# Kernel optimization log

Hardware: AMD Instinct MI355X
Metric: run time of the kernel (lower is better)

## Reference

```python
import jax, jax.numpy as jnp
import numpy as np

TRUNC = (24, 24, 24)
OUT = (32, 32, 32)


def setup_inputs() -> dict:
    key = jax.random.key(0)
    x = jax.random.normal(key, (8, 32, 48, 48, 48), dtype=jnp.float32)
    return {"x": x}


def reference(x):
    # "DCT" as implemented in the source: real part of an ortho-normalized 3D FFT
    x_dct = jnp.real(jnp.fft.fftn(x, axes=(2, 3, 4), norm='ortho'))
    # crop to low-frequency corner, zero-pad up to output_size
    x_crop = x_dct[:, :, :TRUNC[0], :TRUNC[1], :TRUNC[2]]
    pad = ((0, 0), (0, 0),
           (0, OUT[0] - TRUNC[0]),
           (0, OUT[1] - TRUNC[1]),
           (0, OUT[2] - TRUNC[2]))
    x_pad = jnp.pad(x_crop, pad)
    # inverse transform on the output_size grid, keep real part
    x_idct = jnp.real(jnp.fft.ifftn(x_pad, axes=(2, 3, 4), norm='ortho'))
    return x_idct
```

## Files before the change

### kernel.cpp

```cpp
#include <hip/hip_runtime.h>
#include <math.h>


#define TWO_PI_48 0.13089969389957470f
#define TWO_PI_32 0.19634954084936207f
#define NORM_F    1.6611664e-05f

typedef _Float16 half8  __attribute__((ext_vector_type(8)));
typedef _Float16 half4v __attribute__((ext_vector_type(4)));
typedef float    f32x4  __attribute__((ext_vector_type(4)));

__device__ _Float16 T1frag[2][3][2][64][8];
__device__ _Float16 T2frag[2][3][2][64][8];
__device__ __align__(16) _Float16 TK2frag[2][4][3][64][8];
__device__ __align__(16) _Float16 MB2frag[2][4][2][64][8];
__device__ __align__(16) _Float16 TB3frag[2][2][2][64][8];

__device__ int g_twdone = 0;

__global__ void k_init_tw() {
  if (g_twdone) return;
  const int idx = blockIdx.x * 256 + threadIdx.x;
  if (idx < 3072) {
    const int j  = idx & 7;
    const int l  = (idx >> 3) & 63;
    const int ks = (idx >> 9) & 1;
    const int t  = idx >> 10;
    const int k  = ks * 32 + (l >> 4) * 8 + j;
    {
      const int m = t * 16 + (l & 15);
      float v = 0.f;
      if (k < 48) {
        const float a = (float)(((m % 24) * k) % 48) * TWO_PI_48;
        v = (m < 24) ? cosf(a) : -sinf(a);
      }
      const _Float16 h = (_Float16)v;
      T1frag[0][t][ks][l][j] = h;
      T1frag[1][t][ks][l][j] = (_Float16)(v - (float)h);
    }
    {
      const int c = t * 16 + (l & 15);
      float v = 0.f;
      if (k < 48) {
        const float a = (float)(((c % 24) * k) % 48) * TWO_PI_48;
        v = (c < 24) ? cosf(a) : sinf(a);
      }
      const _Float16 h = (_Float16)v;
      T2frag[0][t][ks][l][j] = h;
      T2frag[1][t][ks][l][j] = (_Float16)(v - (float)h);
    }
  } else if (idx < 3072 + 6144) {
    const int local = idx - 3072;
    const int j = local & 7, l = (local >> 3) & 63;
    const int rest = local >> 9;
    const int ks = rest % 3, mt = rest / 3;
    const int m   = mt * 16 + (l & 15);
    const int kap = ks * 32 + (l >> 4) * 8 + j;
    const int n1  = kap % 48;
    const bool isVi = kap >= 48;
    const int m1  = m & 31;
    const bool isWi = m >= 32;
    float acc = 0.f;
    for (int k1 = 0; k1 < 24; ++k1) {
      float s32v, c32v, s48v, c48v;
      sincosf((float)((k1 * m1) % 32) * TWO_PI_32, &s32v, &c32v);
      sincosf((float)((k1 * n1) % 48) * TWO_PI_48, &s48v, &c48v);
      acc = fmaf(isWi ? s32v : c32v, isVi ? s48v : c48v, acc);
    }
    const _Float16 h = (_Float16)acc;
    TK2frag[0][mt][ks][l][j] = h;
    TK2frag[1][mt][ks][l][j] = (_Float16)(acc - (float)h);
  } else if (idx < 3072 + 6144 + 4096) {
    const int local = idx - (3072 + 6144);
    const int j = local & 7, l = (local >> 3) & 63;
    const int rest = local >> 9;
    const int ks = rest & 1, mt = rest >> 1;
    const int m   = mt * 16 + (l & 15);
    const int kap = ks * 32 + (l >> 4) * 8 + j;
    float v = 0.f;
    if (kap < 48) {
      const int k2 = kap % 24;
      const int m2 = m & 31;
      float s, c;
      sincosf((float)((k2 * m2) % 32) * TWO_PI_32, &s, &c);
      if (m < 32) v = (kap < 24) ? c : -s;
      else        v = (kap < 24) ? s :  c;
    }
    const _Float16 h = (_Float16)v;
    MB2frag[0][mt][ks][l][j] = h;
    MB2frag[1][mt][ks][l][j] = (_Float16)(v - (float)h);
  } else if (idx < 15360) {
    const int local = idx - (3072 + 6144 + 4096);
    const int j = local & 7, l = (local >> 3) & 63;
    const int rest = local >> 9;
    const int ks = rest & 1, nt = rest >> 1;
    const int m3  = nt * 16 + (l & 15);
    const int kap = ks * 32 + (l >> 4) * 8 + j;
    float v = 0.f;
    if (kap < 48) {
      const int k3 = kap % 24;
      float s, c;
      sincosf((float)((k3 * m3) % 32) * TWO_PI_32, &s, &c);
      v = (kap < 24) ? c : -s;
    }
    const _Float16 h = (_Float16)v;
    TB3frag[0][nt][ks][l][j] = h;
    TB3frag[1][nt][ks][l][j] = (_Float16)(v - (float)h);
  }
}

__device__ inline void split8(const float* qf, half8& h, half8& lo) {
#pragma unroll
  for (int j = 0; j < 8; ++j) {
    const _Float16 hh = (_Float16)qf[j];
    h[j]  = hh;
    lo[j] = (_Float16)(qf[j] - (float)hh);
  }
}

__global__ __launch_bounds__(192) void k_a12_mfma(const float* __restrict__ x,
                                                  float2* __restrict__ V) {
  const int bx   = blockIdx.x;
  const int bc   = blockIdx.y;
  const int tid  = threadIdx.x;
  const int lane = tid & 63;
  const int w    = tid >> 6;

  __shared__ __align__(16) unsigned char arenaA[13824];
  __shared__ __align__(16) unsigned char arenaB[13824];

  half8 t1h[3][2], t1l[3][2];
#pragma unroll
  for (int mt = 0; mt < 3; ++mt)
#pragma unroll
    for (int ks = 0; ks < 2; ++ks) {
      t1h[mt][ks] = *(const half8*)&T1frag[0][mt][ks][lane][0];
      t1l[mt][ks] = *(const half8*)&T1frag[1][mt][ks][lane][0];
    }
  half8 t2h[2], t2l[2];
#pragma unroll
  for (int ks = 0; ks < 2; ++ks) {
    t2h[ks] = *(const half8*)&T2frag[0][w][ks][lane][0];
    t2l[ks] = *(const half8*)&T2frag[1][w][ks][lane][0];
  }

  const int kb   = (lane >> 4) * 8;
  const int c16  = lane & 15;
  const int k2e  = tid % 24;
  const int k30e = (tid / 24) * 3;

  float4 xr0, xr1, xr2;
  {
    const float4* g4 = (const float4*)(x + ((size_t)(bc * 48 + bx * 2)) * 2304);
    xr0 = g4[tid]; xr1 = g4[tid + 192]; xr2 = g4[tid + 384];
  }

#pragma unroll
  for (int g = 0; g < 2; ++g) {
    const int n1 = bx * 2 + g;
    unsigned char* aX = (g == 0) ? arenaA : arenaB;
    unsigned char* aU = (g == 0) ? arenaB : arenaA;
    _Float16* Xh = (_Float16*)aX;
    _Float16* Xl = (_Float16*)(aX + 6912);
    float*    D2 = (float*)aX;
    _Float16* Uh = (_Float16*)aU;
    _Float16* Ul = (_Float16*)(aU + 6912);

    {
      const float4 fr[3] = {xr0, xr1, xr2};
#pragma unroll
      for (int jj = 0; jj < 3; ++jj) {
        const int i4 = tid + 192 * jj;
        const int r = i4 / 12, c4 = i4 % 12;
        const float4 f = fr[jj];
        const _Float16 h0 = (_Float16)f.x, h1 = (_Float16)f.y,
                       h2 = (_Float16)f.z, h3 = (_Float16)f.w;
        const half4v hv = {h0, h1, h2, h3};
        const half4v lv = {(_Float16)(f.x - (float)h0), (_Float16)(f.y - (float)h1),
                           (_Float16)(f.z - (float)h2), (_Float16)(f.w - (float)h3)};
        *(half4v*)&Xh[r * 72 + c4 * 4] = hv;
        *(half4v*)&Xl[r * 72 + c4 * 4] = lv;
      }
    }
    if (tid < 96) {
      _Float16* p = (tid < 48 ? Xh : Xl) + (tid % 48) * 72 + 48;
      *(half8*)&p[0] = (half8){};
      *(half8*)&p[8] = (half8){};
    }
    if (g < 1) {
      const float4* g4 = (const float4*)(x + ((size_t)(bc * 48 + n1 + 1)) * 2304);
      xr0 = g4[tid]; xr1 = g4[tid + 192]; xr2 = g4[tid + 384];
    }
    __syncthreads();

    f32x4 acc0 = {}, acc1 = {}, acc2 = {};
#pragma unroll
    for (int ks = 0; ks < 2; ++ks) {
      const half8 bh = *(const half8*)&Xh[(w * 16 + c16) * 72 + ks * 32 + kb];
      const half8 bl = *(const half8*)&Xl[(w * 16 + c16) * 72 + ks * 32 + kb];
#pragma unroll
      for (int mt = 0; mt < 3; ++mt) {
        f32x4& acc = (mt == 0) ? acc0 : (mt == 1) ? acc1 : acc2;
        acc = __builtin_amdgcn_mfma_f32_16x16x32_f16(t1h[mt][ks], bh, acc, 0, 0, 0);
        acc = __builtin_amdgcn_mfma_f32_16x16x32_f16(t1h[mt][ks], bl, acc, 0, 0, 0);
        acc = __builtin_amdgcn_mfma_f32_16x16x32_f16(t1l[mt][ks], bh, acc, 0, 0, 0);
      }
    }

#pragma unroll
    for (int mt = 0; mt < 3; ++mt) {
      const int r0 = mt * 16 + (lane >> 4) * 4;
      const int cc = w * 16 + c16;
      const f32x4 acc = (mt == 0) ? acc0 : (mt == 1) ? acc1 : acc2;
#pragma unroll
      for (int r = 0; r < 4; ++r) {
        const float v = acc[r];
        const _Float16 h = (_Float16)v;
        Uh[(r0 + r) * 72 + cc] = h;
        Ul[(r0 + r) * 72 + cc] = (_Float16)(v - (float)h);
      }
    }
    if (tid < 96) {
      _Float16* p = (tid < 48 ? Uh : Ul) + (tid % 48) * 72 + 48;
      *(half8*)&p[0] = (half8){};
      *(half8*)&p[8] = (half8){};
    }
    __syncthreads();

    f32x4 d20 = {}, d21 = {}, d22 = {};
#pragma unroll
    for (int ks = 0; ks < 2; ++ks) {
#pragma unroll
      for (int mt = 0; mt < 3; ++mt) {
        const half8 ah = *(const half8*)&Uh[(mt * 16 + c16) * 72 + ks * 32 + kb];
        const half8 al = *(const half8*)&Ul[(mt * 16 + c16) * 72 + ks * 32 + kb];
        f32x4& acc = (mt == 0) ? d20 : (mt == 1) ? d21 : d22;
        acc = __builtin_amdgcn_mfma_f32_16x16x32_f16(ah, t2h[ks], acc, 0, 0, 0);
        acc = __builtin_amdgcn_mfma_f32_16x16x32_f16(ah, t2l[ks], acc, 0, 0, 0);
        acc = __builtin_amdgcn_mfma_f32_16x16x32_f16(al, t2h[ks], acc, 0, 0, 0);
      }
    }

#pragma unroll
    for (int mt = 0; mt < 3; ++mt) {
      const int r0 = mt * 16 + (lane >> 4) * 4;
      const int cc = w * 16 + c16;
      const f32x4 acc = (mt == 0) ? d20 : (mt == 1) ? d21 : d22;
#pragma unroll
      for (int r = 0; r < 4; ++r) D2[(r0 + r) * 68 + cc] = acc[r];
    }
    __syncthreads();

    float2* Vp = V + (size_t)(bc * 24) * 1152 + (size_t)n1 * 24 + k2e;
#pragma unroll
    for (int q = 0; q < 3; ++q) {
      const int k3 = k30e + q;
      const float grr = D2[k3 * 68 + k2e];
      const float gis = D2[(k3 + 24) * 68 + k2e + 24];
      const float gir = D2[(k3 + 24) * 68 + k2e];
      const float grs = D2[k3 * 68 + k2e + 24];
      Vp[(size_t)k3 * 1152] = make_float2(grr + gis, gir - grs);
    }
  }
}

__global__ __launch_bounds__(192) void k2_mfma(const float2* __restrict__ V,
                                               float2* __restrict__ W) {
  const int k3   = blockIdx.x;
  const int byy  = blockIdx.y;
  const int tid  = threadIdx.x;
  const int lane = tid & 63;
  const int w    = tid >> 6;

  __shared__ __align__(16) float Bb[48 * 100];

  half8 kth[4][3], ktl[4][3];
#pragma unroll
  for (int mt = 0; mt < 4; ++mt)
#pragma unroll
    for (int ks = 0; ks < 3; ++ks) {
      kth[mt][ks] = *(const half8*)&TK2frag[0][mt][ks][lane][0];
      ktl[mt][ks] = *(const half8*)&TK2frag[1][mt][ks][lane][0];
    }

  const int kbase = (lane >> 4) * 8;
  const int c16   = lane & 15;
  const int cc    = w * 16 + c16;
  const int sE    = cc / 24, k2E = cc % 24;
  const int rbase = (lane >> 4) * 4;

  float4 vr[6];
  {
    const float4* g0 = (const float4*)(V + ((size_t)((byy * 4 + 0) * 24 + k3)) * 1152);
    const float4* g1 = (const float4*)(V + ((size_t)((byy * 4 + 1) * 24 + k3)) * 1152);
#pragma unroll
    for (int jj = 0; jj < 6; ++jj)
      vr[jj] = (jj < 3 ? g0 : g1)[tid + 192 * (jj % 3)];
  }

  for (int g = 0; g < 2; ++g) {
    const int bcp = byy * 2 + g;

    if (g) __syncthreads();

#pragma unroll
    for (int jj = 0; jj < 6; ++jj) {
      const int s = jj / 3;
      const int r = tid + 192 * (jj % 3);
      const int n1 = r / 12, c4 = r % 12;
      const float4 f = vr[jj];
      float* bp = &Bb[(s * 24 + c4 * 2) * 100 + n1];
      bp[0]   = f.x;  bp[48]  = f.y;
      bp[100] = f.z;  bp[148] = f.w;
    }
    if (g < 1) {
      const float4* g0 = (const float4*)(V + ((size_t)((bcp * 2 + 2) * 24 + k3)) * 1152);
      const float4* g1 = (const float4*)(V + ((size_t)((bcp * 2 + 3) * 24 + k3)) * 1152);
#pragma unroll
      for (int jj = 0; jj < 6; ++jj)
        vr[jj] = (jj < 3 ? g0 : g1)[tid + 192 * (jj % 3)];
    }
    __syncthreads();

    f32x4 a0 = {}, a1 = {}, a2 = {}, a3 = {};
#pragma unroll
    for (int ks = 0; ks < 3; ++ks) {
      const float4 q0 = *(const float4*)&Bb[cc * 100 + ks * 32 + kbase];
      const float4 q1 = *(const float4*)&Bb[cc * 100 + ks * 32 + kbase + 4];
      const float qf[8] = {q0.x, q0.y, q0.z, q0.w, q1.x, q1.y, q1.z, q1.w};
      half8 bh, bl;
      split8(qf, bh, bl);
#pragma unroll
      for (int mt = 0; mt < 4; ++mt) {
        f32x4& acc = (mt == 0) ? a0 : (mt == 1) ? a1 : (mt == 2) ? a2 : a3;
        acc = __builtin_amdgcn_mfma_f32_16x16x32_f16(kth[mt][ks], bh, acc, 0, 0, 0);
        acc = __builtin_amdgcn_mfma_f32_16x16x32_f16(kth[mt][ks], bl, acc, 0, 0, 0);
        acc = __builtin_amdgcn_mfma_f32_16x16x32_f16(ktl[mt][ks], bh, acc, 0, 0, 0);
      }
    }

    const int bc = bcp * 2 + sE;
    float2* wp = W + (size_t)bc * 18432 + (size_t)k3 * 24 + k2E;
#pragma unroll
    for (int mt = 0; mt < 2; ++mt) {
      const f32x4 wr = (mt == 0) ? a0 : a1;
      const f32x4 wi = (mt == 0) ? a2 : a3;
#pragma unroll
      for (int r = 0; r < 4; ++r) {
        const int m1 = mt * 16 + rbase + r;
        wp[(size_t)m1 * 576] = make_float2(wr[r], wi[r]);
      }
    }
  }
}

__global__ __launch_bounds__(128) void k3_mfma(const float2* __restrict__ W,
                                               float* __restrict__ out) {
  const int m1   = blockIdx.x;
  const int byy  = blockIdx.y;
  const int tid  = threadIdx.x;
  const int lane = tid & 63;
  const int w    = tid >> 6;

  __shared__ __align__(16) float Bt[32 * 68];
  __shared__ __align__(16) float Zb[32 * 68];

  half8 mbh[4][2], mbl[4][2];
#pragma unroll
  for (int mt = 0; mt < 4; ++mt)
#pragma unroll
    for (int ks = 0; ks < 2; ++ks) {
      mbh[mt][ks] = *(const half8*)&MB2frag[0][mt][ks][lane][0];
      mbl[mt][ks] = *(const half8*)&MB2frag[1][mt][ks][lane][0];
    }
  half8 tb3h[2], tb3l[2];
#pragma unroll
  for (int ks = 0; ks < 2; ++ks) {
    tb3h[ks] = *(const half8*)&TB3frag[0][w][ks][lane][0];
    tb3l[ks] = *(const half8*)&TB3frag[1][w][ks][lane][0];
  }

  for (int i = tid; i < 8 * 68; i += 128)  Bt[(24 + i / 68) * 68 + (i % 68)] = 0.f;
  for (int i = tid; i < 24 * 20; i += 128) Bt[(i / 20) * 68 + 48 + (i % 20)] = 0.f;
  for (int i = tid; i < 32 * 20; i += 128) Zb[(i / 20) * 68 + 48 + (i % 20)] = 0.f;

  const int kbase = (lane >> 4) * 8;
  const int c16   = lane & 15;
  const int cc    = w * 16 + c16;
  const int rbase = (lane >> 4) * 4;

  float4 vr0, vr1, vr2;
  {
    const float4* g4 = (const float4*)(W + (size_t)(byy * 2) * 18432 + (size_t)m1 * 576);
    vr0 = g4[tid];
    vr1 = g4[tid + 128];
    if (tid < 32) vr2 = g4[tid + 256];
  }

  for (int g = 0; g < 2; ++g) {
    const int bc = byy * 2 + g;

    {
      const float4 fr[3] = {vr0, vr1, vr2};
#pragma unroll
      for (int jj = 0; jj < 3; ++jj) {
        const int i4 = tid + 128 * jj;
        if (jj < 2 || tid < 32) {
          const int k3 = i4 / 12, c4 = i4 % 12;
          const float4 f = fr[jj];
          Bt[k3 * 68 + 2 * c4]          = f.x;
          Bt[k3 * 68 + 24 + 2 * c4]     = f.y;
          Bt[k3 * 68 + 2 * c4 + 1]      = f.z;
          Bt[k3 * 68 + 24 + 2 * c4 + 1] = f.w;
        }
      }
    }
    if (g < 1) {
      const float4* g4 = (const float4*)(W + (size_t)(bc + 1) * 18432 + (size_t)m1 * 576);
      vr0 = g4[tid];
      vr1 = g4[tid + 128];
      if (tid < 32) vr2 = g4[tid + 256];
    }
    __syncthreads();

    f32x4 z0 = {}, z1 = {}, z2 = {}, z3 = {};
#pragma unroll
    for (int ks = 0; ks < 2; ++ks) {
      const float4 q0 = *(const float4*)&Bt[cc * 68 + ks * 32 + kbase];
      const float4 q1 = *(const float4*)&Bt[cc * 68 + ks * 32 + kbase + 4];
      const float qf[8] = {q0.x, q0.y, q0.z, q0.w, q1.x, q1.y, q1.z, q1.w};
      half8 bh, bl;
      split8(qf, bh, bl);
#pragma unroll
      for (int mt = 0; mt < 4; ++mt) {
        f32x4& acc = (mt == 0) ? z0 : (mt == 1) ? z1 : (mt == 2) ? z2 : z3;
        acc = __builtin_amdgcn_mfma_f32_16x16x32_f16(mbh[mt][ks], bh, acc, 0, 0, 0);
        acc = __builtin_amdgcn_mfma_f32_16x16x32_f16(mbh[mt][ks], bl, acc, 0, 0, 0);
        acc = __builtin_amdgcn_mfma_f32_16x16x32_f16(mbl[mt][ks], bh, acc, 0, 0, 0);
      }
    }
    if (cc < 24) {
#pragma unroll
      for (int mt = 0; mt < 4; ++mt) {
        const f32x4 acc = (mt == 0) ? z0 : (mt == 1) ? z1 : (mt == 2) ? z2 : z3;
        const int row0 = mt * 16 + rbase;
#pragma unroll
        for (int r = 0; r < 4; ++r) {
          const int row = row0 + r;
          if (row < 32) Zb[row * 68 + cc]              = acc[r];
          else          Zb[(row - 32) * 68 + 24 + cc]  = acc[r];
        }
      }
    }
    __syncthreads();

    f32x4 o0 = {}, o1 = {};
#pragma unroll
    for (int ks = 0; ks < 2; ++ks) {
#pragma unroll
      for (int mt = 0; mt < 2; ++mt) {
        const float4 q0 = *(const float4*)&Zb[(mt * 16 + c16) * 68 + ks * 32 + kbase];
        const float4 q1 = *(const float4*)&Zb[(mt * 16 + c16) * 68 + ks * 32 + kbase + 4];
        const float qf[8] = {q0.x, q0.y, q0.z, q0.w, q1.x, q1.y, q1.z, q1.w};
        half8 ah, al;
        split8(qf, ah, al);
        f32x4& acc = (mt == 0) ? o0 : o1;
        acc = __builtin_amdgcn_mfma_f32_16x16x32_f16(ah, tb3h[ks], acc, 0, 0, 0);
        acc = __builtin_amdgcn_mfma_f32_16x16x32_f16(ah, tb3l[ks], acc, 0, 0, 0);
        acc = __builtin_amdgcn_mfma_f32_16x16x32_f16(al, tb3h[ks], acc, 0, 0, 0);
      }
    }
    float* op = out + (size_t)(bc * 32 + m1) * 1024;
#pragma unroll
    for (int mt = 0; mt < 2; ++mt) {
      const f32x4 acc = (mt == 0) ? o0 : o1;
#pragma unroll
      for (int r = 0; r < 4; ++r) {
        const int m2 = mt * 16 + rbase + r;
        op[m2 * 32 + cc] = acc[r] * NORM_F;
      }
    }
  }

  if (tid == 0 && blockIdx.x == 0 && blockIdx.y == 0) g_twdone = 1;
}

extern "C" void kernel_launch(void* const* d_in, const int* in_sizes, int n_in,
                              void* d_out, int out_size, void* d_ws, size_t ws_size,
                              hipStream_t stream) {
  const float* x = (const float*)d_in[0];
  float* out = (float*)d_out;
  float2* V = (float2*)d_ws;
  float2* W = (float2*)((char*)d_ws + 56623104);

  k_init_tw  <<<dim3(60), dim3(256), 0, stream>>>();
  k_a12_mfma <<<dim3(24, 256), dim3(192), 0, stream>>>(x, V);
  k2_mfma    <<<dim3(24, 64), dim3(192), 0, stream>>>(V, W);
  k3_mfma    <<<dim3(32, 128), dim3(128), 0, stream>>>(W, out);
}
```

Baseline: 81.36 us.

## Rewrite first transform stage as single-wave per-slab kernel loading x directly into registers

Replaces the 192-thread block that processed two slabs with a one-wave block per (n1, bc) slab. The input slab is loaded from global memory straight into MFMA B-operand registers and split into fp16 hi/lo pairs, which removes the shared-memory staging of x and the block barriers. The single wave then runs all 3x3 output tiles of the second matmul with twiddles held in registers. This increases block count and register pressure, gives up the prefetch overlap between two slabs, and uses uncoalesced 48-float row-strided loads.

```diff
diff --git a/kernel.cpp b/kernel.cpp
--- a/kernel.cpp
+++ b/kernel.cpp
@@ -118,86 +118,75 @@
   }
 }
 
-__global__ __launch_bounds__(192) void k_a12_mfma(const float* __restrict__ x,
+__global__ __launch_bounds__(64) void k1_waveslab(const float* __restrict__ x,
                                                   float2* __restrict__ V) {
-  const int bx   = blockIdx.x;
+  const int n1   = blockIdx.x;
   const int bc   = blockIdx.y;
-  const int tid  = threadIdx.x;
-  const int lane = tid & 63;
-  const int w    = tid >> 6;
-
-  __shared__ __align__(16) unsigned char arenaA[13824];
-  __shared__ __align__(16) unsigned char arenaB[13824];
-
-  half8 t1h[3][2], t1l[3][2];
+  const int lane = threadIdx.x;
+
+  __shared__ __align__(16) unsigned char arena[13824];
+  _Float16* Uh = (_Float16*)arena;
+  _Float16* Ul = (_Float16*)(arena + 6912);
+  float*    D2 = (float*)arena;
+
+  const int c16  = lane & 15;
+  const int kgrp = lane >> 4;
+  const int kb   = kgrp * 8;
+
+  half8 t1h[3][2], t1l[3][2], t2h[3][2], t2l[3][2];
 #pragma unroll
   for (int mt = 0; mt < 3; ++mt)
 #pragma unroll
     for (int ks = 0; ks < 2; ++ks) {
       t1h[mt][ks] = *(const half8*)&T1frag[0][mt][ks][lane][0];
       t1l[mt][ks] = *(const half8*)&T1frag[1][mt][ks][lane][0];
-    }
-  half8 t2h[2], t2l[2];
-#pragma unroll
-  for (int ks = 0; ks < 2; ++ks) {
-    t2h[ks] = *(const half8*)&T2frag[0][w][ks][lane][0];
-    t2l[ks] = *(const half8*)&T2frag[1][w][ks][lane][0];
-  }
-
-  const int kb   = (lane >> 4) * 8;
-  const int c16  = lane & 15;
-  const int k2e  = tid % 24;
-  const int k30e = (tid / 24) * 3;
-
-  float4 xr0, xr1, xr2;
+      t2h[mt][ks] = *(const half8*)&T2frag[0][mt][ks][lane][0];
+      t2l[mt][ks] = *(const half8*)&T2frag[1][mt][ks][lane][0];
+    }
+
+#pragma unroll
+  for (int p = 0; p < 3; ++p) {
+    const int i = lane + 64 * p;
+    const int which = i / 48, r = i % 48;
+    _Float16* base = (which & 2) ? Ul : Uh;
+    *(half8*)&base[r * 72 + 48 + (which & 1) * 8] = (half8){};
+  }
+
+  const float* xs = x + (size_t)(bc * 48 + n1) * 2304;
+
+  float4 fa0, fb0, fa1, fb1;
   {
-    const float4* g4 = (const float4*)(x + ((size_t)(bc * 48 + bx * 2)) * 2304);
-    xr0 = g4[tid]; xr1 = g4[tid + 192]; xr2 = g4[tid + 384];
-  }
-
-#pragma unroll
-  for (int g = 0; g < 2; ++g) {
-    const int n1 = bx * 2 + g;
-    unsigned char* aX = (g == 0) ? arenaA : arenaB;
-    unsigned char* aU = (g == 0) ? arenaB : arenaA;
-    _Float16* Xh = (_Float16*)aX;
-    _Float16* Xl = (_Float16*)(aX + 6912);
-    float*    D2 = (float*)aX;
-    _Float16* Uh = (_Float16*)aU;
-    _Float16* Ul = (_Float16*)(aU + 6912);
-
-    {
-      const float4 fr[3] = {xr0, xr1, xr2};
-#pragma unroll
-      for (int jj = 0; jj < 3; ++jj) {
-        const int i4 = tid + 192 * jj;
-        const int r = i4 / 12, c4 = i4 % 12;
-        const float4 f = fr[jj];
-        const _Float16 h0 = (_Float16)f.x, h1 = (_Float16)f.y,
-                       h2 = (_Float16)f.z, h3 = (_Float16)f.w;
-        const half4v hv = {h0, h1, h2, h3};
-        const half4v lv = {(_Float16)(f.x - (float)h0), (_Float16)(f.y - (float)h1),
-                           (_Float16)(f.z - (float)h2), (_Float16)(f.w - (float)h3)};
-        *(half4v*)&Xh[r * 72 + c4 * 4] = hv;
-        *(half4v*)&Xl[r * 72 + c4 * 4] = lv;
-      }
-    }
-    if (tid < 96) {
-      _Float16* p = (tid < 48 ? Xh : Xl) + (tid % 48) * 72 + 48;
-      *(half8*)&p[0] = (half8){};
-      *(half8*)&p[8] = (half8){};
-    }
-    if (g < 1) {
-      const float4* g4 = (const float4*)(x + ((size_t)(bc * 48 + n1 + 1)) * 2304);
-      xr0 = g4[tid]; xr1 = g4[tid + 192]; xr2 = g4[tid + 384];
-    }
-    __syncthreads();
+    const float4* p0 = (const float4*)(xs + c16 * 48 + kb);
+    fa0 = p0[0]; fb0 = p0[1];
+    const int k1i = 32 + kb;
+    if (k1i < 48) {
+      const float4* p1 = (const float4*)(xs + c16 * 48 + k1i);
+      fa1 = p1[0]; fb1 = p1[1];
+    } else { fa1 = make_float4(0.f,0.f,0.f,0.f); fb1 = fa1; }
+  }
+
+#pragma unroll
+  for (int nt = 0; nt < 3; ++nt) {
+    float4 na0, nb0, na1, nb1;
+    if (nt < 2) {
+      const int c = (nt + 1) * 16 + c16;
+      const float4* p0 = (const float4*)(xs + c * 48 + kb);
+      na0 = p0[0]; nb0 = p0[1];
+      const int k1i = 32 + kb;
+      if (k1i < 48) {
+        const float4* p1 = (const float4*)(xs + c * 48 + k1i);
+        na1 = p1[0]; nb1 = p1[1];
+      } else { na1 = make_float4(0.f,0.f,0.f,0.f); nb1 = na1; }
+    }
 
     f32x4 acc0 = {}, acc1 = {}, acc2 = {};
 #pragma unroll
     for (int ks = 0; ks < 2; ++ks) {
-      const half8 bh = *(const half8*)&Xh[(w * 16 + c16) * 72 + ks * 32 + kb];
-      const half8 bl = *(const half8*)&Xl[(w * 16 + c16) * 72 + ks * 32 + kb];
+      const float4 qa = ks ? fa1 : fa0;
+      const float4 qb = ks ? fb1 : fb0;
+      const float qf[8] = {qa.x, qa.y, qa.z, qa.w, qb.x, qb.y, qb.z, qb.w};
+      half8 bh, bl;
+      split8(qf, bh, bl);
 #pragma unroll
       for (int mt = 0; mt < 3; ++mt) {
         f32x4& acc = (mt == 0) ? acc0 : (mt == 1) ? acc1 : acc2;
@@ -207,60 +196,62 @@
       }
     }
 
+    {
+      const int cc = nt * 16 + c16;
+#pragma unroll
+      for (int mt = 0; mt < 3; ++mt) {
+        const int r0 = mt * 16 + kgrp * 4;
+        const f32x4 acc = (mt == 0) ? acc0 : (mt == 1) ? acc1 : acc2;
+#pragma unroll
+        for (int r = 0; r < 4; ++r) {
+          const float v = acc[r];
+          const _Float16 h = (_Float16)v;
+          Uh[(r0 + r) * 72 + cc] = h;
+          Ul[(r0 + r) * 72 + cc] = (_Float16)(v - (float)h);
+        }
+      }
+    }
+
+    fa0 = na0; fb0 = nb0; fa1 = na1; fb1 = nb1;
+  }
+
+  f32x4 a2[3][3] = {};
+#pragma unroll
+  for (int ks = 0; ks < 2; ++ks) {
 #pragma unroll
     for (int mt = 0; mt < 3; ++mt) {
-      const int r0 = mt * 16 + (lane >> 4) * 4;
-      const int cc = w * 16 + c16;
-      const f32x4 acc = (mt == 0) ? acc0 : (mt == 1) ? acc1 : acc2;
-#pragma unroll
-      for (int r = 0; r < 4; ++r) {
-        const float v = acc[r];
-        const _Float16 h = (_Float16)v;
-        Uh[(r0 + r) * 72 + cc] = h;
-        Ul[(r0 + r) * 72 + cc] = (_Float16)(v - (float)h);
-      }
-    }
-    if (tid < 96) {
-      _Float16* p = (tid < 48 ? Uh : Ul) + (tid % 48) * 72 + 48;
-      *(half8*)&p[0] = (half8){};
-      *(half8*)&p[8] = (half8){};
-    }
-    __syncthreads();
-
-    f32x4 d20 = {}, d21 = {}, d22 = {};
-#pragma unroll
-    for (int ks = 0; ks < 2; ++ks) {
-#pragma unroll
-      for (int mt = 0; mt < 3; ++mt) {
-        const half8 ah = *(const half8*)&Uh[(mt * 16 + c16) * 72 + ks * 32 + kb];
-        const half8 al = *(const half8*)&Ul[(mt * 16 + c16) * 72 + ks * 32 + kb];
-        f32x4& acc = (mt == 0) ? d20 : (mt == 1) ? d21 : d22;
-        acc = __builtin_amdgcn_mfma_f32_16x16x32_f16(ah, t2h[ks], acc, 0, 0, 0);
-        acc = __builtin_amdgcn_mfma_f32_16x16x32_f16(ah, t2l[ks], acc, 0, 0, 0);
-        acc = __builtin_amdgcn_mfma_f32_16x16x32_f16(al, t2h[ks], acc, 0, 0, 0);
-      }
-    }
-
-#pragma unroll
-    for (int mt = 0; mt < 3; ++mt) {
-      const int r0 = mt * 16 + (lane >> 4) * 4;
-      const int cc = w * 16 + c16;
-      const f32x4 acc = (mt == 0) ? d20 : (mt == 1) ? d21 : d22;
-#pragma unroll
-      for (int r = 0; r < 4; ++r) D2[(r0 + r) * 68 + cc] = acc[r];
-    }
-    __syncthreads();
-
-    float2* Vp = V + (size_t)(bc * 24) * 1152 + (size_t)n1 * 24 + k2e;
-#pragma unroll
-    for (int q = 0; q < 3; ++q) {
-      const int k3 = k30e + q;
-      const float grr = D2[k3 * 68 + k2e];
-      const float gis = D2[(k3 + 24) * 68 + k2e + 24];
-      const float gir = D2[(k3 + 24) * 68 + k2e];
-      const float grs = D2[k3 * 68 + k2e + 24];
-      Vp[(size_t)k3 * 1152] = make_float2(grr + gis, gir - grs);
-    }
+      const half8 ah = *(const half8*)&Uh[(mt * 16 + c16) * 72 + ks * 32 + kb];
+      const half8 al = *(const half8*)&Ul[(mt * 16 + c16) * 72 + ks * 32 + kb];
+#pragma unroll
+      for (int nt2 = 0; nt2 < 3; ++nt2) {
+        a2[mt][nt2] = __builtin_amdgcn_mfma_f32_16x16x32_f16(ah, t2h[nt2][ks], a2[mt][nt2], 0, 0, 0);
+        a2[mt][nt2] = __builtin_amdgcn_mfma_f32_16x16x32_f16(ah, t2l[nt2][ks], a2[mt][nt2], 0, 0, 0);
+        a2[mt][nt2] = __builtin_amdgcn_mfma_f32_16x16x32_f16(al, t2h[nt2][ks], a2[mt][nt2], 0, 0, 0);
+      }
+    }
+  }
+
+#pragma unroll
+  for (int mt = 0; mt < 3; ++mt)
+#pragma unroll
+    for (int nt2 = 0; nt2 < 3; ++nt2) {
+      const int r0 = mt * 16 + kgrp * 4;
+      const int cc = nt2 * 16 + c16;
+#pragma unroll
+      for (int r = 0; r < 4; ++r)
+        D2[(r0 + r) * 68 + cc] = a2[mt][nt2][r];
+    }
+
+#pragma unroll
+  for (int q = 0; q < 9; ++q) {
+    const int idx = lane + 64 * q;
+    const int k3 = idx / 24, k2 = idx % 24;
+    const float grr = D2[k3 * 68 + k2];
+    const float gis = D2[(k3 + 24) * 68 + k2 + 24];
+    const float gir = D2[(k3 + 24) * 68 + k2];
+    const float grs = D2[k3 * 68 + k2 + 24];
+    V[(size_t)bc * 27648 + (size_t)k3 * 1152 + n1 * 24 + k2] =
+        make_float2(grr + gis, gir - grs);
   }
 }
 
@@ -493,8 +484,8 @@
   float2* V = (float2*)d_ws;
   float2* W = (float2*)((char*)d_ws + 56623104);
 
-  k_init_tw  <<<dim3(60), dim3(256), 0, stream>>>();
-  k_a12_mfma <<<dim3(24, 256), dim3(192), 0, stream>>>(x, V);
-  k2_mfma    <<<dim3(24, 64), dim3(192), 0, stream>>>(V, W);
-  k3_mfma    <<<dim3(32, 128), dim3(128), 0, stream>>>(W, out);
-}
+  k_init_tw   <<<dim3(60), dim3(256), 0, stream>>>();
+  k1_waveslab <<<dim3(48, 256), dim3(64), 0, stream>>>(x, V);
+  k2_mfma     <<<dim3(24, 64), dim3(192), 0, stream>>>(V, W);
+  k3_mfma     <<<dim3(32, 128), dim3(128), 0, stream>>>(W, out);
+}
```

Result: no change. 80.11 us (-1.5%).
